# Performance work log

Measured on AMD Instinct MI355X. Metric: run time of the kernel, lower is better.

The kernel has to match this reference:

```python
import jax, jax.numpy as jnp
import numpy as np

N_NODES = 50000
N_EDGES = 800000
NEG_SLOPE = 0.2  # leaky_relu slope used in the model


def setup_inputs() -> dict:
    key = jax.random.key(0)
    ks = jax.random.split(key, 8)
    d_in, d_h, d_out = 64, 64, 4
    x = jax.random.normal(ks[0], (N_NODES, d_in), dtype=jnp.float32)
    edge_index = jax.random.randint(ks[1], (2, N_EDGES), 0, N_NODES, dtype=jnp.int32)
    # Glorot-style init like PyG GCNConv
    W0 = jax.random.normal(ks[2], (d_in, d_h), dtype=jnp.float32) * np.float32(1.0 / np.sqrt(d_in))
    W1 = jax.random.normal(ks[3], (d_h, d_h), dtype=jnp.float32) * np.float32(1.0 / np.sqrt(d_h))
    W2 = jax.random.normal(ks[4], (d_h, d_out), dtype=jnp.float32) * np.float32(1.0 / np.sqrt(d_h))
    b0 = jnp.zeros((d_h,), dtype=jnp.float32)
    b1 = jnp.zeros((d_h,), dtype=jnp.float32)
    b2 = jnp.zeros((d_out,), dtype=jnp.float32)
    return {"x": x, "edge_index": edge_index, "W0": W0, "b0": b0,
            "W1": W1, "b1": b1, "W2": W2, "b2": b2}


def _gcn_norm(edge_index, n_nodes, dtype):
    # Add self-loops, compute symmetric normalization D^{-1/2} (A+I) D^{-1/2}
    src, dst = edge_index[0], edge_index[1]
    loop = jnp.arange(n_nodes, dtype=src.dtype)
    src = jnp.concatenate([src, loop])
    dst = jnp.concatenate([dst, loop])
    deg = jax.ops.segment_sum(jnp.ones_like(dst, dtype=dtype), dst, num_segments=n_nodes)
    dinv = jnp.where(deg > 0, jax.lax.rsqrt(deg), jnp.zeros_like(deg))
    norm = dinv[src] * dinv[dst]  # [E + N]
    return src, dst, norm


def _gcn_layer(h, src, dst, norm, W, b, n_nodes):
    h = h @ W                                  # [N, d_out]
    msg = h[src] * norm[:, None]               # gather + edge scaling
    out = jax.ops.segment_sum(msg, dst, num_segments=n_nodes)  # scatter-add
    return out + b


def reference(x, edge_index, W0, b0, W1, b1, W2, b2):
    # Eval-mode forward: dropout_edge and F.dropout are identity when not training.
    n = x.shape[0]
    src, dst, norm = _gcn_norm(edge_index, n, x.dtype)
    h = _gcn_layer(x, src, dst, norm, W0, b0, n)
    h = jax.nn.leaky_relu(h, NEG_SLOPE)
    h = _gcn_layer(h, src, dst, norm, W1, b1, n)
    h = jax.nn.leaky_relu(h, NEG_SLOPE)
    out = _gcn_layer(h, src, dst, norm, W2, b2, n)
    return out
```

## Files before the change

### kernel.cpp

```cpp
#include <hip/hip_runtime.h>
#include <math.h>

#define NEG_SLOPE 0.2f
#define NPAD 50176
#define NW8  (NPAD / 4)
#define NCHUNK 256

typedef _Float16 half4 __attribute__((ext_vector_type(4)));

__global__ __launch_bounds__(1024) void k_hist(const int* __restrict__ dst,
                                               unsigned int* __restrict__ histw,
                                               int e, int es) {
    extern __shared__ unsigned int lcnt[];
    int t = threadIdx.x;
    for (int w = t; w < NW8; w += 1024) lcnt[w] = 0u;
    __syncthreads();
    int beg = blockIdx.x * es;
    int end = min(beg + es, e);
    for (int i = beg + t; i < end; i += 1024) {
        int d = dst[i];
        atomicAdd(&lcnt[d >> 2], 1u << ((d & 3) << 3));
    }
    __syncthreads();
    unsigned int* out = histw + (size_t)blockIdx.x * NW8;
    for (int w = t; w < NW8; w += 1024) out[w] = lcnt[w];
}

__global__ __launch_bounds__(256) void k_chscan(unsigned char* __restrict__ hist8,
                                                float* __restrict__ dinv,
                                                unsigned short* __restrict__ deg16,
                                                int* __restrict__ bsum, int n) {
    int t = threadIdx.x;
    int i = blockIdx.x * 256 + t;
    unsigned char* p = hist8 + i;
    unsigned int run = 0;
    for (int c = 0; c < NCHUNK; c += 8) {
        size_t b = (size_t)c * NPAD;
        unsigned char v0 = p[b];
        unsigned char v1 = p[b + (size_t)1 * NPAD];
        unsigned char v2 = p[b + (size_t)2 * NPAD];
        unsigned char v3 = p[b + (size_t)3 * NPAD];
        unsigned char v4 = p[b + (size_t)4 * NPAD];
        unsigned char v5 = p[b + (size_t)5 * NPAD];
        unsigned char v6 = p[b + (size_t)6 * NPAD];
        unsigned char v7 = p[b + (size_t)7 * NPAD];
        unsigned int e0 = run;
        unsigned int e1 = e0 + v0;
        unsigned int e2 = e1 + v1;
        unsigned int e3 = e2 + v2;
        unsigned int e4 = e3 + v3;
        unsigned int e5 = e4 + v4;
        unsigned int e6 = e5 + v5;
        unsigned int e7 = e6 + v6;
        run = e7 + v7;
        p[b] = (unsigned char)e0;
        p[b + (size_t)1 * NPAD] = (unsigned char)e1;
        p[b + (size_t)2 * NPAD] = (unsigned char)e2;
        p[b + (size_t)3 * NPAD] = (unsigned char)e3;
        p[b + (size_t)4 * NPAD] = (unsigned char)e4;
        p[b + (size_t)5 * NPAD] = (unsigned char)e5;
        p[b + (size_t)6 * NPAD] = (unsigned char)e6;
        p[b + (size_t)7 * NPAD] = (unsigned char)e7;
    }
    int deg = (int)run;
    if (i < n) dinv[i] = rsqrtf((float)(deg + 1));
    deg16[i] = (unsigned short)deg;
    int s = deg;
    for (int d = 1; d < 64; d <<= 1) s += __shfl_down(s, d);
    __shared__ int ws[4];
    if ((t & 63) == 0) ws[t >> 6] = s;
    __syncthreads();
    if (t == 0) bsum[blockIdx.x] = ws[0] + ws[1] + ws[2] + ws[3];
}

__global__ __launch_bounds__(256) void k_scan3(const unsigned short* __restrict__ deg16,
                                               const int* __restrict__ bsum,
                                               int* __restrict__ rowptr, int n, int nb) {
    __shared__ int ls[256];
    __shared__ int wo[4];
    int t = threadIdx.x;
    int bid = blockIdx.x;
    int bv = (t < bid && t < nb) ? bsum[t] : 0;
    for (int d = 1; d < 64; d <<= 1) bv += __shfl_down(bv, d);
    if ((t & 63) == 0) wo[t >> 6] = bv;
    __syncthreads();
    int boff = wo[0] + wo[1] + wo[2] + wo[3];
    int i = bid * 256 + t;
    int v = (i < n) ? (int)deg16[i] : 0;
    ls[t] = v;
    __syncthreads();
    for (int d = 1; d < 256; d <<= 1) {
        int u = (t >= d) ? ls[t - d] : 0;
        __syncthreads();
        ls[t] += u;
        __syncthreads();
    }
    int excl = ls[t] - v + boff;
    if (i < n) rowptr[i] = excl;
    if (i == n - 1) rowptr[n] = excl + v;
}

__global__ __launch_bounds__(1024) void k_place2(const int* __restrict__ src,
                                                 const int* __restrict__ dst,
                                                 const int* __restrict__ rowptr,
                                                 const unsigned int* __restrict__ choffw,
                                                 int* __restrict__ perm, int e, int es) {
    extern __shared__ unsigned int cur[];
    int t = threadIdx.x;
    const unsigned int* in = choffw + (size_t)blockIdx.x * NW8;
    for (int w = t; w < NW8; w += 1024) cur[w] = in[w];
    __syncthreads();
    int beg = blockIdx.x * es;
    int end = min(beg + es, e);
    for (int i = beg + t; i < end; i += 1024) {
        int d = dst[i];
        int sh = (d & 3) << 3;
        unsigned int old = atomicAdd(&cur[d >> 2], 1u << sh);
        int slot = rowptr[d] + (int)((old >> sh) & 0xffu);
        perm[slot] = src[i];
    }
}

template <typename T>
__global__ __launch_bounds__(256) void k_gemm64(const T* __restrict__ in,
                                                const float* __restrict__ W,
                                                const float* __restrict__ dinv,
                                                _Float16* __restrict__ out, int n) {
    __shared__ float Ws[64 * 64];
    __shared__ float Xs[16 * 64];
    int t = threadIdx.x;
    const float4* W4 = (const float4*)W;
    float4* Ws4 = (float4*)Ws;
#pragma unroll
    for (int i = 0; i < 4; ++i) Ws4[t + 256 * i] = W4[t + 256 * i];
    int row0 = blockIdx.x * 16;
    {
        int r = t >> 4, c4 = t & 15;
        int row = row0 + r;
        float4 v = make_float4(0.f, 0.f, 0.f, 0.f);
        if (row < n) {
            if constexpr (sizeof(T) == 4) {
                v = ((const float4*)(in + (size_t)row * 64))[c4];
            } else {
                half4 hv = ((const half4*)(in + (size_t)row * 64))[c4];
                v = make_float4((float)hv.x, (float)hv.y, (float)hv.z, (float)hv.w);
            }
        }
        ((float4*)Xs)[t] = v;
    }
    __syncthreads();
    int c = t & 63, g = t >> 6;
    float a0 = 0.f, a1 = 0.f, a2 = 0.f, a3 = 0.f;
#pragma unroll
    for (int k = 0; k < 64; ++k) {
        float w = Ws[k * 64 + c];
        a0 = fmaf(Xs[g * 64 + k], w, a0);
        a1 = fmaf(Xs[(g + 4) * 64 + k], w, a1);
        a2 = fmaf(Xs[(g + 8) * 64 + k], w, a2);
        a3 = fmaf(Xs[(g + 12) * 64 + k], w, a3);
    }
    int r;
    r = row0 + g;      if (r < n) out[(size_t)r * 64 + c] = (_Float16)(a0 * dinv[r]);
    r = row0 + g + 4;  if (r < n) out[(size_t)r * 64 + c] = (_Float16)(a1 * dinv[r]);
    r = row0 + g + 8;  if (r < n) out[(size_t)r * 64 + c] = (_Float16)(a2 * dinv[r]);
    r = row0 + g + 12; if (r < n) out[(size_t)r * 64 + c] = (_Float16)(a3 * dinv[r]);
}

__global__ __launch_bounds__(256) void k_gather64(
        const _Float16* __restrict__ h, const float* __restrict__ dinv,
        const int* __restrict__ rowptr, const int* __restrict__ perm,
        const float* __restrict__ b, _Float16* __restrict__ out, int n, int act,
        const float* __restrict__ W2, float* __restrict__ y, int fuse) {
    int t = threadIdx.x;
    int v = blockIdx.x * 4 + (t >> 6);
    if (v >= n) return;
    v = __builtin_amdgcn_readfirstlane(v);
    int lane = t & 63;
    const _Float16* hl = h + lane;
    float acc = (float)hl[(size_t)v * 64];
    int e = rowptr[v], end = rowptr[v + 1];
#define LOADK(j) float x##j = (float)hl[(size_t)perm[e + j] * 64]
    for (; e + 16 <= end; e += 16) {
        LOADK(0); LOADK(1); LOADK(2); LOADK(3);
        LOADK(4); LOADK(5); LOADK(6); LOADK(7);
        LOADK(8); LOADK(9); LOADK(10); LOADK(11);
        LOADK(12); LOADK(13); LOADK(14); LOADK(15);
        acc += (((x0 + x1) + (x2 + x3)) + ((x4 + x5) + (x6 + x7)))
             + (((x8 + x9) + (x10 + x11)) + ((x12 + x13) + (x14 + x15)));
    }
    if (e + 8 <= end) {
        LOADK(0); LOADK(1); LOADK(2); LOADK(3);
        LOADK(4); LOADK(5); LOADK(6); LOADK(7);
        acc += ((x0 + x1) + (x2 + x3)) + ((x4 + x5) + (x6 + x7));
        e += 8;
    }
    if (e + 4 <= end) {
        LOADK(0); LOADK(1); LOADK(2); LOADK(3);
        acc += (x0 + x1) + (x2 + x3);
        e += 4;
    }
    if (e + 2 <= end) {
        LOADK(0); LOADK(1);
        acc += x0 + x1;
        e += 2;
    }
    if (e < end) acc += (float)hl[(size_t)perm[e] * 64];
#undef LOADK
    float dv = dinv[v];
    acc = acc * dv + b[lane];
    if (act) acc = acc > 0.0f ? acc : acc * NEG_SLOPE;
    if (!fuse) {
        out[(size_t)v * 64 + lane] = (_Float16)acc;
    } else {
        float4 w = ((const float4*)W2)[lane];
        float p0 = acc * w.x, p1 = acc * w.y, p2 = acc * w.z, p3 = acc * w.w;
#pragma unroll
        for (int dlt = 1; dlt < 64; dlt <<= 1) {
            p0 += __shfl_xor(p0, dlt);
            p1 += __shfl_xor(p1, dlt);
            p2 += __shfl_xor(p2, dlt);
            p3 += __shfl_xor(p3, dlt);
        }
        if (lane == 0)
            ((float4*)y)[v] = make_float4(p0 * dv, p1 * dv, p2 * dv, p3 * dv);
    }
}

__global__ __launch_bounds__(256) void k_gather4(
        const float* __restrict__ h, const float* __restrict__ dinv,
        const int* __restrict__ rowptr, const int* __restrict__ perm,
        const float* __restrict__ b, float* __restrict__ out, int n) {
    int gid = blockIdx.x * 256 + threadIdx.x;
    int c = gid & 3;
    int v = gid >> 2;
    if (v >= n) return;
    const float* hc = h + c;
    float acc = hc[(size_t)v * 4];
    int e = rowptr[v], end = rowptr[v + 1];
    for (; e + 4 <= end; e += 4) {
        float x0 = hc[(size_t)perm[e] * 4];
        float x1 = hc[(size_t)perm[e + 1] * 4];
        float x2 = hc[(size_t)perm[e + 2] * 4];
        float x3 = hc[(size_t)perm[e + 3] * 4];
        acc += (x0 + x1) + (x2 + x3);
    }
    for (; e < end; ++e) acc += hc[(size_t)perm[e] * 4];
    out[(size_t)v * 4 + c] = acc * dinv[v] + b[c];
}

extern "C" void kernel_launch(void* const* d_in, const int* in_sizes, int n_in,
                              void* d_out, int out_size, void* d_ws, size_t ws_size,
                              hipStream_t stream) {
    const float* x  = (const float*)d_in[0];
    const int* ei   = (const int*)d_in[1];
    const float* W0 = (const float*)d_in[2];
    const float* b0 = (const float*)d_in[3];
    const float* W1 = (const float*)d_in[4];
    const float* b1 = (const float*)d_in[5];
    const float* W2 = (const float*)d_in[6];
    const float* b2 = (const float*)d_in[7];
    float* out = (float*)d_out;

    const int N = in_sizes[0] / 64;
    const int E = in_sizes[1] / 2;
    const int* src = ei;
    const int* dst = ei + E;
    const int es = (E + NCHUNK - 1) / NCHUNK;

    char* base = (char*)d_ws;
    size_t off = 0;
    auto alloc = [&](size_t bytes) { size_t o = off; off = (off + bytes + 255) & ~(size_t)255; return o; };
    unsigned int*   histw  = (unsigned int*)(base + alloc((size_t)NCHUNK * NPAD));
    unsigned short* deg16  = (unsigned short*)(base + alloc((size_t)NPAD * 2));
    float*          dinv   = (float*)(base + alloc((size_t)NPAD * 4));
    int*            rowptr = (int*)(base + alloc((size_t)(NPAD + 1) * 4));
    int*            bsum   = (int*)(base + alloc(1024));
    int*            perm   = (int*)(base + alloc((size_t)E * 4));
    _Float16*       bufH   = (_Float16*)(base + alloc((size_t)N * 64 * 2));
    _Float16*       bufB16 = (_Float16*)(base + alloc((size_t)N * 64 * 2));
    float*          bufD   = (float*)(base + alloc((size_t)N * 4 * 4));

    const int nb_N = (N + 255) / 256;
    const int nb_V = (N + 3) / 4;

    k_hist<<<NCHUNK, 1024, NW8 * sizeof(unsigned int), stream>>>(dst, histw, E, es);
    k_chscan<<<NPAD / 256, 256, 0, stream>>>((unsigned char*)histw, dinv, deg16, bsum, N);
    k_scan3<<<nb_N, 256, 0, stream>>>(deg16, bsum, rowptr, N, nb_N);
    k_place2<<<NCHUNK, 1024, NW8 * sizeof(unsigned int), stream>>>(src, dst, rowptr, histw, perm, E, es);

    k_gemm64<float><<<(N + 15) / 16, 256, 0, stream>>>(x, W0, dinv, bufH, N);
    k_gather64<<<nb_V, 256, 0, stream>>>(bufH, dinv, rowptr, perm, b0, bufB16, N, 1,
                                         W2, bufD, 0);

    k_gemm64<_Float16><<<(N + 15) / 16, 256, 0, stream>>>(bufB16, W1, dinv, bufH, N);
    k_gather64<<<nb_V, 256, 0, stream>>>(bufH, dinv, rowptr, perm, b1, bufB16, N, 1,
                                         W2, bufD, 1);

    k_gather4<<<(N * 4 + 255) / 256, 256, 0, stream>>>(bufD, dinv, rowptr, perm, b2, out, N);
}
```

Before: 159.5 us.

## Fuse layer-1 aggregation with layer-2 GEMM in a single kernel

Adds a kernel that gathers neighbor features for 16 nodes per 1024-thread block, applies bias and leaky ReLU into shared memory, then multiplies by W1 in the same block. This removes one kernel launch and the fp16 round-trip of the intermediate activation through global memory. In exchange, the 1024-thread blocks wait on a barrier for their slowest node before the GEMM phase, and only a quarter of the threads do the GEMM, which may reduce occupancy and latency hiding in the gather phase.

```diff
diff --git a/kernel.cpp b/kernel.cpp
--- a/kernel.cpp
+++ b/kernel.cpp
@@ -121,8 +121,7 @@
     }
 }
 
-template <typename T>
-__global__ __launch_bounds__(256) void k_gemm64(const T* __restrict__ in,
+__global__ __launch_bounds__(256) void k_gemm64(const float* __restrict__ in,
                                                 const float* __restrict__ W,
                                                 const float* __restrict__ dinv,
                                                 _Float16* __restrict__ out, int n) {
@@ -138,14 +137,7 @@
         int r = t >> 4, c4 = t & 15;
         int row = row0 + r;
         float4 v = make_float4(0.f, 0.f, 0.f, 0.f);
-        if (row < n) {
-            if constexpr (sizeof(T) == 4) {
-                v = ((const float4*)(in + (size_t)row * 64))[c4];
-            } else {
-                half4 hv = ((const half4*)(in + (size_t)row * 64))[c4];
-                v = make_float4((float)hv.x, (float)hv.y, (float)hv.z, (float)hv.w);
-            }
-        }
+        if (row < n) v = ((const float4*)(in + (size_t)row * 64))[c4];
         ((float4*)Xs)[t] = v;
     }
     __syncthreads();
@@ -166,11 +158,81 @@
     r = row0 + g + 12; if (r < n) out[(size_t)r * 64 + c] = (_Float16)(a3 * dinv[r]);
 }
 
+__global__ __launch_bounds__(1024) void k_gather_gemm(
+        const _Float16* __restrict__ h, const float* __restrict__ dinv,
+        const int* __restrict__ rowptr, const int* __restrict__ perm,
+        const float* __restrict__ b, const float* __restrict__ W,
+        _Float16* __restrict__ out, int n) {
+    __shared__ float Ws[64 * 64];
+    __shared__ float Xs[16 * 64];
+    int t = threadIdx.x;
+    ((float4*)Ws)[t] = ((const float4*)W)[t];
+    int row0 = blockIdx.x * 16;
+    int wid = t >> 6;
+    int lane = t & 63;
+    int v = row0 + wid;
+    if (v < n) {
+        v = __builtin_amdgcn_readfirstlane(v);
+        const _Float16* hl = h + lane;
+        float acc = (float)hl[(size_t)v * 64];
+        int e = rowptr[v], end = rowptr[v + 1];
+#define LOADK(j) float x##j = (float)hl[(size_t)perm[e + j] * 64]
+        for (; e + 16 <= end; e += 16) {
+            LOADK(0); LOADK(1); LOADK(2); LOADK(3);
+            LOADK(4); LOADK(5); LOADK(6); LOADK(7);
+            LOADK(8); LOADK(9); LOADK(10); LOADK(11);
+            LOADK(12); LOADK(13); LOADK(14); LOADK(15);
+            acc += (((x0 + x1) + (x2 + x3)) + ((x4 + x5) + (x6 + x7)))
+                 + (((x8 + x9) + (x10 + x11)) + ((x12 + x13) + (x14 + x15)));
+        }
+        if (e + 8 <= end) {
+            LOADK(0); LOADK(1); LOADK(2); LOADK(3);
+            LOADK(4); LOADK(5); LOADK(6); LOADK(7);
+            acc += ((x0 + x1) + (x2 + x3)) + ((x4 + x5) + (x6 + x7));
+            e += 8;
+        }
+        if (e + 4 <= end) {
+            LOADK(0); LOADK(1); LOADK(2); LOADK(3);
+            acc += (x0 + x1) + (x2 + x3);
+            e += 4;
+        }
+        if (e + 2 <= end) {
+            LOADK(0); LOADK(1);
+            acc += x0 + x1;
+            e += 2;
+        }
+        if (e < end) acc += (float)hl[(size_t)perm[e] * 64];
+#undef LOADK
+        float dv = dinv[v];
+        acc = acc * dv + b[lane];
+        acc = acc > 0.0f ? acc : acc * NEG_SLOPE;
+        Xs[wid * 64 + lane] = acc;
+    }
+    __syncthreads();
+    if (t < 256) {
+        int c = t & 63, g = t >> 6;
+        float a0 = 0.f, a1 = 0.f, a2 = 0.f, a3 = 0.f;
+#pragma unroll
+        for (int k = 0; k < 64; ++k) {
+            float w = Ws[k * 64 + c];
+            a0 = fmaf(Xs[g * 64 + k], w, a0);
+            a1 = fmaf(Xs[(g + 4) * 64 + k], w, a1);
+            a2 = fmaf(Xs[(g + 8) * 64 + k], w, a2);
+            a3 = fmaf(Xs[(g + 12) * 64 + k], w, a3);
+        }
+        int r;
+        r = row0 + g;      if (r < n) out[(size_t)r * 64 + c] = (_Float16)(a0 * dinv[r]);
+        r = row0 + g + 4;  if (r < n) out[(size_t)r * 64 + c] = (_Float16)(a1 * dinv[r]);
+        r = row0 + g + 8;  if (r < n) out[(size_t)r * 64 + c] = (_Float16)(a2 * dinv[r]);
+        r = row0 + g + 12; if (r < n) out[(size_t)r * 64 + c] = (_Float16)(a3 * dinv[r]);
+    }
+}
+
 __global__ __launch_bounds__(256) void k_gather64(
         const _Float16* __restrict__ h, const float* __restrict__ dinv,
         const int* __restrict__ rowptr, const int* __restrict__ perm,
-        const float* __restrict__ b, _Float16* __restrict__ out, int n, int act,
-        const float* __restrict__ W2, float* __restrict__ y, int fuse) {
+        const float* __restrict__ b, int n,
+        const float* __restrict__ W2, float* __restrict__ y) {
     int t = threadIdx.x;
     int v = blockIdx.x * 4 + (t >> 6);
     if (v >= n) return;
@@ -208,22 +270,18 @@
 #undef LOADK
     float dv = dinv[v];
     acc = acc * dv + b[lane];
-    if (act) acc = acc > 0.0f ? acc : acc * NEG_SLOPE;
-    if (!fuse) {
-        out[(size_t)v * 64 + lane] = (_Float16)acc;
-    } else {
-        float4 w = ((const float4*)W2)[lane];
-        float p0 = acc * w.x, p1 = acc * w.y, p2 = acc * w.z, p3 = acc * w.w;
+    acc = acc > 0.0f ? acc : acc * NEG_SLOPE;
+    float4 w = ((const float4*)W2)[lane];
+    float p0 = acc * w.x, p1 = acc * w.y, p2 = acc * w.z, p3 = acc * w.w;
 #pragma unroll
-        for (int dlt = 1; dlt < 64; dlt <<= 1) {
-            p0 += __shfl_xor(p0, dlt);
-            p1 += __shfl_xor(p1, dlt);
-            p2 += __shfl_xor(p2, dlt);
-            p3 += __shfl_xor(p3, dlt);
-        }
-        if (lane == 0)
-            ((float4*)y)[v] = make_float4(p0 * dv, p1 * dv, p2 * dv, p3 * dv);
-    }
+    for (int dlt = 1; dlt < 64; dlt <<= 1) {
+        p0 += __shfl_xor(p0, dlt);
+        p1 += __shfl_xor(p1, dlt);
+        p2 += __shfl_xor(p2, dlt);
+        p3 += __shfl_xor(p3, dlt);
+    }
+    if (lane == 0)
+        ((float4*)y)[v] = make_float4(p0 * dv, p1 * dv, p2 * dv, p3 * dv);
 }
 
 __global__ __launch_bounds__(256) void k_gather4(
@@ -277,24 +335,23 @@
     int*            bsum   = (int*)(base + alloc(1024));
     int*            perm   = (int*)(base + alloc((size_t)E * 4));
     _Float16*       bufH   = (_Float16*)(base + alloc((size_t)N * 64 * 2));
-    _Float16*       bufB16 = (_Float16*)(base + alloc((size_t)N * 64 * 2));
+    _Float16*       bufH2  = (_Float16*)(base + alloc((size_t)N * 64 * 2));
     float*          bufD   = (float*)(base + alloc((size_t)N * 4 * 4));
 
     const int nb_N = (N + 255) / 256;
     const int nb_V = (N + 3) / 4;
+    const int nb_F = (N + 15) / 16;
 
     k_hist<<<NCHUNK, 1024, NW8 * sizeof(unsigned int), stream>>>(dst, histw, E, es);
     k_chscan<<<NPAD / 256, 256, 0, stream>>>((unsigned char*)histw, dinv, deg16, bsum, N);
     k_scan3<<<nb_N, 256, 0, stream>>>(deg16, bsum, rowptr, N, nb_N);
     k_place2<<<NCHUNK, 1024, NW8 * sizeof(unsigned int), stream>>>(src, dst, rowptr, histw, perm, E, es);
 
-    k_gemm64<float><<<(N + 15) / 16, 256, 0, stream>>>(x, W0, dinv, bufH, N);
-    k_gather64<<<nb_V, 256, 0, stream>>>(bufH, dinv, rowptr, perm, b0, bufB16, N, 1,
-                                         W2, bufD, 0);
-
-    k_gemm64<_Float16><<<(N + 15) / 16, 256, 0, stream>>>(bufB16, W1, dinv, bufH, N);
-    k_gather64<<<nb_V, 256, 0, stream>>>(bufH, dinv, rowptr, perm, b1, bufB16, N, 1,
-                                         W2, bufD, 1);
+    k_gemm64<<<nb_F, 256, 0, stream>>>(x, W0, dinv, bufH, N);
+
+    k_gather_gemm<<<nb_F, 1024, 0, stream>>>(bufH, dinv, rowptr, perm, b0, W1, bufH2, N);
+
+    k_gather64<<<nb_V, 256, 0, stream>>>(bufH2, dinv, rowptr, perm, b1, N, W2, bufD);
 
     k_gather4<<<(N * 4 + 255) / 256, 256, 0, stream>>>(bufD, dinv, rowptr, perm, b2, out, N);
 }
```

New measurement: 383.6 us. 2.41x slower.
